# Kernel tuning notes

Hardware: AMD Instinct MI355X
Metric: run time of the kernel (lower is better)

Reference implementation:

```python
import jax, jax.numpy as jnp
from jax import lax
import numpy as np

INPUT_DIMS = 512
HIDDEN_DIMS = 1024
OUTPUT_DIMS = 512
BATCH = 64
T = 256


def setup_inputs() -> dict:
    key = jax.random.key(0)
    ks = jax.random.split(key, 9)
    s_ih = 1.0 / np.sqrt(HIDDEN_DIMS)
    inp = {
        "x": jax.random.normal(ks[0], (BATCH, INPUT_DIMS, T), dtype=jnp.float32),
        # LSTMCell params (PyTorch gate order: i, f, g, o)
        "W_ih": jax.random.uniform(ks[1], (4 * HIDDEN_DIMS, INPUT_DIMS), minval=-s_ih, maxval=s_ih, dtype=jnp.float32),
        "W_hh": jax.random.uniform(ks[2], (4 * HIDDEN_DIMS, HIDDEN_DIMS), minval=-s_ih, maxval=s_ih, dtype=jnp.float32),
        "b_ih": jax.random.uniform(ks[3], (4 * HIDDEN_DIMS,), minval=-s_ih, maxval=s_ih, dtype=jnp.float32),
        "b_hh": jax.random.uniform(ks[4], (4 * HIDDEN_DIMS,), minval=-s_ih, maxval=s_ih, dtype=jnp.float32),
        # Output linear
        "W_out": jax.random.uniform(ks[5], (OUTPUT_DIMS, HIDDEN_DIMS), minval=-s_ih, maxval=s_ih, dtype=jnp.float32),
        "b_out": jax.random.uniform(ks[6], (OUTPUT_DIMS,), minval=-s_ih, maxval=s_ih, dtype=jnp.float32),
        # Initial state (learned-ish constants in the original, sampled from randn)
        "h0": jax.random.normal(ks[7], (1, HIDDEN_DIMS), dtype=jnp.float32),
        "c0": jax.random.normal(ks[8], (1, HIDDEN_DIMS), dtype=jnp.float32),
    }
    return inp


def reference(x, W_ih, W_hh, b_ih, b_hh, W_out, b_out, h0, c0):
    B, I, Tlen = x.shape
    H = W_hh.shape[1]
    h = jnp.broadcast_to(h0, (B, H))
    c = jnp.broadcast_to(c0, (B, H))
    xs = jnp.transpose(x, (2, 0, 1))  # [T, B, I]
    # Precompute the input projection for all timesteps in one GEMM.
    x_proj = jnp.einsum("tbi,gi->tbg", xs, W_ih) + b_ih  # [T, B, 4H]

    def step(carry, xp):
        h, c = carry
        gates = xp + h @ W_hh.T + b_hh  # [B, 4H]
        i_g, f_g, g_g, o_g = jnp.split(gates, 4, axis=-1)
        i_g = jax.nn.sigmoid(i_g)
        f_g = jax.nn.sigmoid(f_g)
        g_g = jnp.tanh(g_g)
        o_g = jax.nn.sigmoid(o_g)
        c_new = f_g * c + i_g * g_g
        h_new = o_g * jnp.tanh(c_new)
        # NOTE: original applies the output head to the CELL state c, not h.
        p = jax.nn.softmax(c_new @ W_out.T + b_out, axis=1)  # [B, O]
        return (h_new, c_new), p

    _, ps = lax.scan(step, (h, c), x_proj)  # ps: [T, B, O]
    # torch.cat along dim 0 per timestep == stack then flatten first two dims.
    return ps.reshape(Tlen * B, -1)
```

## Files before the change

kernel.cpp:

```cpp
#include <hip/hip_runtime.h>


#define T_ 256

typedef __attribute__((ext_vector_type(8))) short bf16x8;
typedef __attribute__((ext_vector_type(4))) float floatx4;
typedef __attribute__((ext_vector_type(4))) int intx4;

__device__ __forceinline__ unsigned short f2bf(float f) {
  unsigned u = __builtin_bit_cast(unsigned, f);
  u += 0x7FFFu + ((u >> 16) & 1u);
  return (unsigned short)(u >> 16);
}

__device__ __forceinline__ float sigm(float x) { return 1.0f / (1.0f + __expf(-x)); }
__device__ __forceinline__ float tanh_fast(float x) {
  return __builtin_fmaf(2.f, sigm(2.f * x), -1.f);
}

__global__ void cvt_w(const float* __restrict__ w, unsigned short* __restrict__ o) {
  const size_t g = (size_t)blockIdx.x * 256 + threadIdx.x;
  const float* s = w + g * 8;
  bf16x8 v;
#pragma unroll
  for (int i = 0; i < 8; ++i) v[i] = (short)f2bf(s[i]);
  *(bf16x8*)(o + g * 8) = v;
}

__global__ void transpose_x(const float* __restrict__ x, unsigned short* __restrict__ xT) {
  __shared__ float tile[32][33];
  const int b = blockIdx.z, i0 = blockIdx.y * 32, t0 = blockIdx.x * 32;
  const int tx = threadIdx.x & 31, ty = threadIdx.x >> 5;
#pragma unroll
  for (int p = 0; p < 4; ++p) {
    const int i = ty + p * 8;
    tile[i][tx] = x[((size_t)b * 512 + i0 + i) * 256 + t0 + tx];
  }
  __syncthreads();
#pragma unroll
  for (int p = 0; p < 4; ++p) {
    const int t = ty + p * 8;
    xT[((size_t)(t0 + t) * 64 + b) * 512 + i0 + tx] = f2bf(tile[tx][t]);
  }
}

__global__ __launch_bounds__(512, 1) void lstm_rec(
    const float* __restrict__ Whh, const float* __restrict__ Wih,
    const float* __restrict__ bih, const float* __restrict__ bhh,
    const float* __restrict__ h0, const float* __restrict__ c0,
    const unsigned short* __restrict__ xT,
    unsigned short* __restrict__ hbuf,
    unsigned short* __restrict__ call)
{
  const int tid = threadIdx.x;
  const int lane = tid & 63;
  const int wv = tid >> 6;
  const int nh = wv & 1, kq = wv >> 1;
  const int mg = blockIdx.x & 3, ng = blockIdx.x >> 2;
  const int l15 = lane & 15, lq = lane >> 4;
  const int row = mg * 16 + l15;

  __shared__ unsigned short hlds[16 * 1032];
  __shared__ float gpart[4][16][66];

  bf16x8 bfrag[2][12];
#pragma unroll
  for (int nt = 0; nt < 2; ++nt) {
    const int ncol = (2 * nh + nt) * 1024 + ng * 16 + l15;
#pragma unroll
    for (int ks = 0; ks < 12; ++ks) {
      const int kg = kq * 384 + ks * 32 + lq * 8;
      const float* s = (kg < 1024) ? (Whh + (size_t)ncol * 1024 + kg)
                                   : (Wih + (size_t)ncol * 512 + (kg - 1024));
      bf16x8 v;
#pragma unroll
      for (int i = 0; i < 8; ++i) v[i] = (short)f2bf(s[i]);
      bfrag[nt][ks] = v;
    }
  }

  const int m_loc = tid >> 4, j = tid & 15;
  const int row_g = mg * 16 + m_loc;
  const int unit = ng * 16 + j;
  float c_reg = 0.f, bs0 = 0.f, bs1 = 0.f, bs2 = 0.f, bs3 = 0.f;
  if (tid < 256) {
    c_reg = c0[unit];
    bs0 = bih[unit] + bhh[unit];
    bs1 = bih[1024 + unit] + bhh[1024 + unit];
    bs2 = bih[2048 + unit] + bhh[2048 + unit];
    bs3 = bih[3072 + unit] + bhh[3072 + unit];
  }

  for (int t = 0; t < T_; ++t) {
    const unsigned short* bx = xT + ((size_t)t * 64 + row) * 512;
    floatx4 zero = {0.f, 0.f, 0.f, 0.f};
    floatx4 acc0 = zero, acc1 = zero;

#pragma unroll
    for (int ks = 0; ks < 12; ++ks) {
      const int kg = kq * 384 + ks * 32 + lq * 8;
      if (kg >= 1024) {
        const bf16x8 af = *(const bf16x8*)(bx + (kg - 1024));
        acc0 = __builtin_amdgcn_mfma_f32_16x16x32_bf16(af, bfrag[0][ks], acc0, 0, 0, 0);
        acc1 = __builtin_amdgcn_mfma_f32_16x16x32_bf16(af, bfrag[1][ks], acc1, 0, 0, 0);
      }
    }

    if (t == 0) {
#pragma unroll
      for (int p = 0; p < 4; ++p) {
        const int e = tid + p * 512;
        const int r = e >> 7, col = (e & 127) * 8;
        const float* s = h0 + col;
        bf16x8 v;
#pragma unroll
        for (int i = 0; i < 8; ++i) v[i] = (short)f2bf(s[i]);
        *(bf16x8*)(hlds + r * 1032 + col) = v;
      }
      __syncthreads();
    } else {
      const unsigned short* hprev = hbuf + ((t + 1) & 1) * 65536;
      const unsigned tagpat = (((t - 1) >> 1) & 1) ? 0x40004000u : 0u;

      if (wv == 0) {
        const unsigned short* ssrc = hprev + (size_t)(mg * 16) * 1024 + (size_t)lane * 16;
        while (true) {
          intx4 s0;
          asm volatile("global_load_dwordx4 %0, %1, off sc0 sc1\n\ts_waitcnt vmcnt(0)"
                       : "=v"(s0) : "v"(ssrc) : "memory");
          unsigned bad = 0;
#pragma unroll
          for (int d = 0; d < 4; ++d) bad |= ((unsigned)s0[d] ^ tagpat) & 0x40004000u;
          if (__all(bad == 0)) break;
          __builtin_amdgcn_s_sleep(1);
        }
      }
      __syncthreads();

      const unsigned short* gsrc = hprev + (size_t)(mg * 16) * 1024 + (size_t)tid * 8;
      intx4 a0, a1, a2, a3;
      while (true) {
        asm volatile(
            "global_load_dwordx4 %0, %4, off sc0 sc1\n\t"
            "global_load_dwordx4 %1, %5, off sc0 sc1\n\t"
            "global_load_dwordx4 %2, %6, off sc0 sc1\n\t"
            "global_load_dwordx4 %3, %7, off sc0 sc1\n\t"
            "s_waitcnt vmcnt(0)"
            : "=v"(a0), "=v"(a1), "=v"(a2), "=v"(a3)
            : "v"(gsrc), "v"(gsrc + 4096), "v"(gsrc + 8192), "v"(gsrc + 12288)
            : "memory");
        unsigned bad = 0;
#pragma unroll
        for (int d = 0; d < 4; ++d) {
          bad |= ((unsigned)a0[d] ^ tagpat) & 0x40004000u;
          bad |= ((unsigned)a1[d] ^ tagpat) & 0x40004000u;
          bad |= ((unsigned)a2[d] ^ tagpat) & 0x40004000u;
          bad |= ((unsigned)a3[d] ^ tagpat) & 0x40004000u;
        }
        if (!bad) break;
        __builtin_amdgcn_s_sleep(1);
      }
      intx4 av[4] = {a0, a1, a2, a3};
#pragma unroll
      for (int p = 0; p < 4; ++p) {
        intx4 v = av[p];
#pragma unroll
        for (int d = 0; d < 4; ++d) v[d] &= (int)0xBFFFBFFFu;
        const int e = tid + p * 512;
        const int r = e >> 7, col = (e & 127) * 8;
        *(intx4*)(hlds + r * 1032 + col) = v;
      }
      __syncthreads();
    }

#pragma unroll
    for (int ks = 0; ks < 12; ++ks) {
      const int kg = kq * 384 + ks * 32 + lq * 8;
      if (kg < 1024) {
        const bf16x8 af = *(const bf16x8*)(hlds + l15 * 1032 + kg);
        acc0 = __builtin_amdgcn_mfma_f32_16x16x32_bf16(af, bfrag[0][ks], acc0, 0, 0, 0);
        acc1 = __builtin_amdgcn_mfma_f32_16x16x32_bf16(af, bfrag[1][ks], acc1, 0, 0, 0);
      }
    }

#pragma unroll
    for (int r = 0; r < 4; ++r) {
      gpart[kq][lq * 4 + r][(2 * nh) * 16 + l15]     = acc0[r];
      gpart[kq][lq * 4 + r][(2 * nh + 1) * 16 + l15] = acc1[r];
    }
    __syncthreads();

    if (tid < 256) {
      float gi = bs0, gf = bs1, gg = bs2, go = bs3;
#pragma unroll
      for (int q = 0; q < 4; ++q) {
        gi += gpart[q][m_loc][j];
        gf += gpart[q][m_loc][16 + j];
        gg += gpart[q][m_loc][32 + j];
        go += gpart[q][m_loc][48 + j];
      }
      const float iv = sigm(gi), fv = sigm(gf), gv = tanh_fast(gg), ov = sigm(go);
      c_reg = fv * c_reg + iv * gv;
      const float hv = ov * tanh_fast(c_reg);

      const unsigned hb = (unsigned)f2bf(hv) | ((unsigned)((t >> 1) & 1) << 14);
      const int base = lane & 56;
      intx4 pk;
#pragma unroll
      for (int k = 0; k < 4; ++k) {
        const unsigned lo = (unsigned)__shfl((int)hb, base + 2 * k, 64) & 0xFFFFu;
        const unsigned hi = (unsigned)__shfl((int)hb, base + 2 * k + 1, 64);
        pk[k] = (int)(lo | (hi << 16));
      }
      if ((tid & 7) == 0) {
        unsigned short* hp = hbuf + (t & 1) * 65536 + row_g * 1024 + (unit & ~7);
        asm volatile("global_store_dwordx4 %0, %1, off sc0 sc1"
                     :: "v"(hp), "v"(pk) : "memory");
      }
      call[((size_t)t * 64 + row_g) * 1024 + unit] = f2bf(c_reg);
    }
  }
}

__global__ __launch_bounds__(256, 1) void lstm_head(
    const unsigned short* __restrict__ call,
    const unsigned short* __restrict__ wout,
    const float* __restrict__ bout,
    float* __restrict__ out)
{
  const int tb = blockIdx.x;
  const int lane = threadIdx.x & 63;
  const int wv = threadIdx.x >> 6;
  const int l15 = lane & 15, lq = lane >> 4;

  __shared__ float sred[2][4][64];

  floatx4 zero = {0.f, 0.f, 0.f, 0.f};
  floatx4 acc[4][8];
#pragma unroll
  for (int mt = 0; mt < 4; ++mt)
#pragma unroll
    for (int nt = 0; nt < 8; ++nt) acc[mt][nt] = zero;

  const unsigned short* abase = call + ((size_t)tb * 64 + l15) * 1024 + lq * 8;
  const unsigned short* bbase = wout + ((size_t)(wv * 128 + l15)) * 1024 + lq * 8;

#pragma unroll 2
  for (int ks = 0; ks < 32; ++ks) {
    bf16x8 a[4];
#pragma unroll
    for (int mt = 0; mt < 4; ++mt)
      a[mt] = *(const bf16x8*)(abase + (size_t)mt * 16 * 1024 + ks * 32);
#pragma unroll
    for (int nt = 0; nt < 8; ++nt) {
      const bf16x8 b = *(const bf16x8*)(bbase + (size_t)nt * 16 * 1024 + ks * 32);
#pragma unroll
      for (int mt = 0; mt < 4; ++mt)
        acc[mt][nt] = __builtin_amdgcn_mfma_f32_16x16x32_bf16(a[mt], b, acc[mt][nt], 0, 0, 0);
    }
  }

#pragma unroll
  for (int nt = 0; nt < 8; ++nt) {
    const float bo = bout[wv * 128 + nt * 16 + l15];
#pragma unroll
    for (int mt = 0; mt < 4; ++mt)
#pragma unroll
      for (int r = 0; r < 4; ++r) acc[mt][nt][r] += bo;
  }

  float rmax[4][4];
#pragma unroll
  for (int mt = 0; mt < 4; ++mt)
#pragma unroll
    for (int r = 0; r < 4; ++r) {
      float m = acc[mt][0][r];
#pragma unroll
      for (int nt = 1; nt < 8; ++nt) m = fmaxf(m, acc[mt][nt][r]);
      m = fmaxf(m, __shfl_xor(m, 1, 64));
      m = fmaxf(m, __shfl_xor(m, 2, 64));
      m = fmaxf(m, __shfl_xor(m, 4, 64));
      m = fmaxf(m, __shfl_xor(m, 8, 64));
      rmax[mt][r] = m;
    }
  if (l15 == 0) {
#pragma unroll
    for (int mt = 0; mt < 4; ++mt)
#pragma unroll
      for (int r = 0; r < 4; ++r) sred[0][wv][mt * 16 + lq * 4 + r] = rmax[mt][r];
  }
  __syncthreads();
  float gmax[4][4], rsum[4][4];
#pragma unroll
  for (int mt = 0; mt < 4; ++mt)
#pragma unroll
    for (int r = 0; r < 4; ++r) {
      const int rw = mt * 16 + lq * 4 + r;
      gmax[mt][r] = fmaxf(fmaxf(sred[0][0][rw], sred[0][1][rw]),
                          fmaxf(sred[0][2][rw], sred[0][3][rw]));
      rsum[mt][r] = 0.f;
    }
#pragma unroll
  for (int mt = 0; mt < 4; ++mt)
#pragma unroll
    for (int nt = 0; nt < 8; ++nt)
#pragma unroll
      for (int r = 0; r < 4; ++r) {
        const float e = __expf(acc[mt][nt][r] - gmax[mt][r]);
        acc[mt][nt][r] = e;
        rsum[mt][r] += e;
      }
#pragma unroll
  for (int mt = 0; mt < 4; ++mt)
#pragma unroll
    for (int r = 0; r < 4; ++r) {
      float s = rsum[mt][r];
      s += __shfl_xor(s, 1, 64);
      s += __shfl_xor(s, 2, 64);
      s += __shfl_xor(s, 4, 64);
      s += __shfl_xor(s, 8, 64);
      rsum[mt][r] = s;
    }
  if (l15 == 0) {
#pragma unroll
    for (int mt = 0; mt < 4; ++mt)
#pragma unroll
      for (int r = 0; r < 4; ++r) sred[1][wv][mt * 16 + lq * 4 + r] = rsum[mt][r];
  }
  __syncthreads();
#pragma unroll
  for (int mt = 0; mt < 4; ++mt)
#pragma unroll
    for (int r = 0; r < 4; ++r) {
      const int rw = mt * 16 + lq * 4 + r;
      const float inv = 1.0f / (sred[1][0][rw] + sred[1][1][rw] +
                                sred[1][2][rw] + sred[1][3][rw]);
      float* orow = out + ((size_t)tb * 64 + rw) * 512 + wv * 128 + l15;
#pragma unroll
      for (int nt = 0; nt < 8; ++nt) orow[nt * 16] = acc[mt][nt][r] * inv;
    }
}

extern "C" void kernel_launch(void* const* d_in, const int* in_sizes, int n_in,
                              void* d_out, int out_size, void* d_ws, size_t ws_size,
                              hipStream_t stream) {
  const float* x    = (const float*)d_in[0];
  const float* Wih  = (const float*)d_in[1];
  const float* Whh  = (const float*)d_in[2];
  const float* bih  = (const float*)d_in[3];
  const float* bhh  = (const float*)d_in[4];
  const float* Wout = (const float*)d_in[5];
  const float* bout = (const float*)d_in[6];
  const float* h0   = (const float*)d_in[7];
  const float* c0   = (const float*)d_in[8];
  float* out = (float*)d_out;

  char* ws = (char*)d_ws;
  unsigned short* hbuf  = (unsigned short*)(ws + 4096);
  unsigned short* woutb = (unsigned short*)(ws + 266240);
  unsigned short* xT    = (unsigned short*)(ws + 1314816);
  unsigned short* call  = (unsigned short*)(ws + 18092032);

  hipMemsetAsync(hbuf, 0xFF, 262144, stream);
  cvt_w<<<256, 256, 0, stream>>>(Wout, woutb);
  transpose_x<<<dim3(8, 16, 64), 256, 0, stream>>>(x, xT);
  lstm_rec<<<256, 512, 0, stream>>>(Whh, Wih, bih, bhh, h0, c0, xT, hbuf, call);
  lstm_head<<<256, 256, 0, stream>>>(call, woutb, bout, out);
}
```

Measured before the change: 1.316 ms.

## Use per-timestep hidden-state ring buffer to avoid tagged double-buffer polling

Adds a mode that writes each timestep's hidden state to its own slot in a 256-entry ring buffer, pre-filled with 0xFF, so readiness is detected by cleared tag bits rather than alternating parity tags. The bulk read now uses plain cached loads, and only chunks that are not yet valid are re-polled with coherent loads. This is meant to cut the cost of the cross-block barrier on each step, in exchange for a 32 MB memset and extra workspace. The old path is kept as a fallback when the workspace is too small.

Measured after the change: 1.219 ms. 1.08x faster.

```diff
diff --git a/kernel.cpp b/kernel.cpp
--- a/kernel.cpp
+++ b/kernel.cpp
@@ -50,7 +50,9 @@
     const float* __restrict__ h0, const float* __restrict__ c0,
     const unsigned short* __restrict__ xT,
     unsigned short* __restrict__ hbuf,
-    unsigned short* __restrict__ call)
+    unsigned short* __restrict__ hring,
+    unsigned short* __restrict__ call,
+    const int mode)
 {
   const int tid = threadIdx.x;
   const int lane = tid & 63;
@@ -118,10 +120,8 @@
         *(bf16x8*)(hlds + r * 1032 + col) = v;
       }
       __syncthreads();
-    } else {
-      const unsigned short* hprev = hbuf + ((t + 1) & 1) * 65536;
-      const unsigned tagpat = (((t - 1) >> 1) & 1) ? 0x40004000u : 0u;
-
+    } else if (mode) {
+      const unsigned short* hprev = hring + (size_t)(t - 1) * 65536;
       if (wv == 0) {
         const unsigned short* ssrc = hprev + (size_t)(mg * 16) * 1024 + (size_t)lane * 16;
         while (true) {
@@ -130,13 +130,58 @@
                        : "=v"(s0) : "v"(ssrc) : "memory");
           unsigned bad = 0;
 #pragma unroll
+          for (int d = 0; d < 4; ++d) bad |= (unsigned)s0[d] & 0x40004000u;
+          if (__all(bad == 0)) break;
+          __builtin_amdgcn_s_sleep(1);
+        }
+      }
+      __syncthreads();
+      const unsigned short* gsrc = hprev + (size_t)(mg * 16) * 1024 + (size_t)tid * 8;
+      intx4 av[4];
+      av[0] = *(const intx4*)(gsrc);
+      av[1] = *(const intx4*)(gsrc + 4096);
+      av[2] = *(const intx4*)(gsrc + 8192);
+      av[3] = *(const intx4*)(gsrc + 12288);
+#pragma unroll
+      for (int p = 0; p < 4; ++p) {
+        unsigned bad = 0;
+#pragma unroll
+        for (int d = 0; d < 4; ++d) bad |= (unsigned)av[p][d] & 0x40004000u;
+        if (bad) {
+          const unsigned short* ptr = gsrc + p * 4096;
+          while (true) {
+            intx4 vv;
+            asm volatile("global_load_dwordx4 %0, %1, off sc0 sc1\n\ts_waitcnt vmcnt(0)"
+                         : "=v"(vv) : "v"(ptr) : "memory");
+            unsigned b2 = 0;
+#pragma unroll
+            for (int d = 0; d < 4; ++d) b2 |= (unsigned)vv[d] & 0x40004000u;
+            if (!b2) { av[p] = vv; break; }
+            __builtin_amdgcn_s_sleep(1);
+          }
+        }
+        const int e = tid + p * 512;
+        const int r = e >> 7, col = (e & 127) * 8;
+        *(intx4*)(hlds + r * 1032 + col) = av[p];
+      }
+      __syncthreads();
+    } else {
+      const unsigned short* hprev = hbuf + ((t + 1) & 1) * 65536;
+      const unsigned tagpat = (((t - 1) >> 1) & 1) ? 0x40004000u : 0u;
+      if (wv == 0) {
+        const unsigned short* ssrc = hprev + (size_t)(mg * 16) * 1024 + (size_t)lane * 16;
+        while (true) {
+          intx4 s0;
+          asm volatile("global_load_dwordx4 %0, %1, off sc0 sc1\n\ts_waitcnt vmcnt(0)"
+                       : "=v"(s0) : "v"(ssrc) : "memory");
+          unsigned bad = 0;
+#pragma unroll
           for (int d = 0; d < 4; ++d) bad |= ((unsigned)s0[d] ^ tagpat) & 0x40004000u;
           if (__all(bad == 0)) break;
           __builtin_amdgcn_s_sleep(1);
         }
       }
       __syncthreads();
-
       const unsigned short* gsrc = hprev + (size_t)(mg * 16) * 1024 + (size_t)tid * 8;
       intx4 a0, a1, a2, a3;
       while (true) {
@@ -160,10 +205,10 @@
         if (!bad) break;
         __builtin_amdgcn_s_sleep(1);
       }
-      intx4 av[4] = {a0, a1, a2, a3};
+      intx4 avv[4] = {a0, a1, a2, a3};
 #pragma unroll
       for (int p = 0; p < 4; ++p) {
-        intx4 v = av[p];
+        intx4 v = avv[p];
 #pragma unroll
         for (int d = 0; d < 4; ++d) v[d] &= (int)0xBFFFBFFFu;
         const int e = tid + p * 512;
@@ -203,7 +248,8 @@
       c_reg = fv * c_reg + iv * gv;
       const float hv = ov * tanh_fast(c_reg);
 
-      const unsigned hb = (unsigned)f2bf(hv) | ((unsigned)((t >> 1) & 1) << 14);
+      const unsigned hb = (unsigned)f2bf(hv)
+                        | (mode ? 0u : ((unsigned)((t >> 1) & 1) << 14));
       const int base = lane & 56;
       intx4 pk;
 #pragma unroll
@@ -213,7 +259,9 @@
         pk[k] = (int)(lo | (hi << 16));
       }
       if ((tid & 7) == 0) {
-        unsigned short* hp = hbuf + (t & 1) * 65536 + row_g * 1024 + (unit & ~7);
+        unsigned short* hp = (mode ? hring + (size_t)t * 65536
+                                   : hbuf + (t & 1) * 65536)
+                             + row_g * 1024 + (unit & ~7);
         asm volatile("global_store_dwordx4 %0, %1, off sc0 sc1"
                      :: "v"(hp), "v"(pk) : "memory");
       }
@@ -360,10 +408,18 @@
   unsigned short* woutb = (unsigned short*)(ws + 266240);
   unsigned short* xT    = (unsigned short*)(ws + 1314816);
   unsigned short* call  = (unsigned short*)(ws + 18092032);
-
-  hipMemsetAsync(hbuf, 0xFF, 262144, stream);
+  unsigned short* hring = (unsigned short*)(ws + 51646464);
+
+  const size_t need = 51646464ull + 33554432ull;
+  const int mode = (ws_size >= need) ? 1 : 0;
+
+  if (mode) {
+    hipMemsetAsync(hring, 0xFF, 33554432, stream);
+  } else {
+    hipMemsetAsync(hbuf, 0xFF, 262144, stream);
+  }
   cvt_w<<<256, 256, 0, stream>>>(Wout, woutb);
   transpose_x<<<dim3(8, 16, 64), 256, 0, stream>>>(x, xT);
-  lstm_rec<<<256, 512, 0, stream>>>(Whh, Wih, bih, bhh, h0, c0, xT, hbuf, call);
+  lstm_rec<<<256, 512, 0, stream>>>(Whh, Wih, bih, bhh, h0, c0, xT, hbuf, hring, call, mode);
   lstm_head<<<256, 256, 0, stream>>>(call, woutb, bout, out);
 }
```

## Repartition recurrence blocks into 8-row groups and add per-step h ring buffer

Applied to the files above, without the earlier changes.

Each block now covers 8 batch rows and 32 hidden units, so every block reads only 8 rows of h per step instead of 16. Each step's h is also written to a per-timestep ring buffer that starts filled with 0xFF, which lets readers poll without tag parity and with a cheaper sc0-only load. The old double-buffered, tagged path stays as a fallback when the workspace is too small or after repeated polling misses. The cost is an extra 32 MB memset, extra global stores every step, half of each MFMA's output rows left unused, and doubled B-fragment register use.

Result: slower. 2.168 ms (+64.8%).

```diff
diff --git a/kernel.cpp b/kernel.cpp
--- a/kernel.cpp
+++ b/kernel.cpp
@@ -2,6 +2,7 @@
 
 
 #define T_ 256
+#define FASTROUNDS 48
 
 typedef __attribute__((ext_vector_type(8))) short bf16x8;
 typedef __attribute__((ext_vector_type(4))) float floatx4;
@@ -50,38 +51,42 @@
     const float* __restrict__ h0, const float* __restrict__ c0,
     const unsigned short* __restrict__ xT,
     unsigned short* __restrict__ hbuf,
-    unsigned short* __restrict__ call)
+    unsigned short* __restrict__ hring,
+    unsigned short* __restrict__ call,
+    const int have_ring)
 {
   const int tid = threadIdx.x;
   const int lane = tid & 63;
   const int wv = tid >> 6;
   const int nh = wv & 1, kq = wv >> 1;
-  const int mg = blockIdx.x & 3, ng = blockIdx.x >> 2;
+  const int xg = blockIdx.x & 7;
+  const int ngb = blockIdx.x >> 3;
   const int l15 = lane & 15, lq = lane >> 4;
-  const int row = mg * 16 + l15;
-
-  __shared__ unsigned short hlds[16 * 1032];
-  __shared__ float gpart[4][16][66];
-
-  bf16x8 bfrag[2][12];
-#pragma unroll
-  for (int nt = 0; nt < 2; ++nt) {
-    const int ncol = (2 * nh + nt) * 1024 + ng * 16 + l15;
+  const int hrow = l15 & 7;
+
+  __shared__ unsigned short hlds[8 * 1032];
+  __shared__ float gpart[4][8][132];
+
+  bf16x8 bfrag[4][12];
+#pragma unroll
+  for (int a = 0; a < 4; ++a) {
+    const int c = nh * 64 + a * 16 + l15;
+    const int wcol = (c >> 5) * 1024 + ngb * 32 + (c & 31);
 #pragma unroll
     for (int ks = 0; ks < 12; ++ks) {
       const int kg = kq * 384 + ks * 32 + lq * 8;
-      const float* s = (kg < 1024) ? (Whh + (size_t)ncol * 1024 + kg)
-                                   : (Wih + (size_t)ncol * 512 + (kg - 1024));
+      const float* s = (kg < 1024) ? (Whh + (size_t)wcol * 1024 + kg)
+                                   : (Wih + (size_t)wcol * 512 + (kg - 1024));
       bf16x8 v;
 #pragma unroll
       for (int i = 0; i < 8; ++i) v[i] = (short)f2bf(s[i]);
-      bfrag[nt][ks] = v;
-    }
-  }
-
-  const int m_loc = tid >> 4, j = tid & 15;
-  const int row_g = mg * 16 + m_loc;
-  const int unit = ng * 16 + j;
+      bfrag[a][ks] = v;
+    }
+  }
+
+  const int m_loc = tid >> 5, j = tid & 31;
+  const int row_g = xg * 8 + m_loc;
+  const int unit = ngb * 32 + j;
   float c_reg = 0.f, bs0 = 0.f, bs1 = 0.f, bs2 = 0.f, bs3 = 0.f;
   if (tid < 256) {
     c_reg = c0[unit];
@@ -91,102 +96,95 @@
     bs3 = bih[3072 + unit] + bhh[3072 + unit];
   }
 
+  int fails = have_ring ? 0 : 1000;
+
   for (int t = 0; t < T_; ++t) {
-    const unsigned short* bx = xT + ((size_t)t * 64 + row) * 512;
     floatx4 zero = {0.f, 0.f, 0.f, 0.f};
-    floatx4 acc0 = zero, acc1 = zero;
-
+    floatx4 acc[4] = {zero, zero, zero, zero};
+
+    const unsigned short* bx = xT + ((size_t)t * 64 + xg * 8 + hrow) * 512;
 #pragma unroll
     for (int ks = 0; ks < 12; ++ks) {
       const int kg = kq * 384 + ks * 32 + lq * 8;
       if (kg >= 1024) {
         const bf16x8 af = *(const bf16x8*)(bx + (kg - 1024));
-        acc0 = __builtin_amdgcn_mfma_f32_16x16x32_bf16(af, bfrag[0][ks], acc0, 0, 0, 0);
-        acc1 = __builtin_amdgcn_mfma_f32_16x16x32_bf16(af, bfrag[1][ks], acc1, 0, 0, 0);
+#pragma unroll
+        for (int a = 0; a < 4; ++a)
+          acc[a] = __builtin_amdgcn_mfma_f32_16x16x32_bf16(af, bfrag[a][ks], acc[a], 0, 0, 0);
       }
     }
 
     if (t == 0) {
 #pragma unroll
-      for (int p = 0; p < 4; ++p) {
-        const int e = tid + p * 512;
-        const int r = e >> 7, col = (e & 127) * 8;
-        const float* s = h0 + col;
+      for (int p = 0; p < 2; ++p) {
+        const int g = tid + p * 512;
+        const int row8 = g >> 7, colu = (g & 127) * 8;
+        const float* s = h0 + colu;
         bf16x8 v;
 #pragma unroll
         for (int i = 0; i < 8; ++i) v[i] = (short)f2bf(s[i]);
-        *(bf16x8*)(hlds + r * 1032 + col) = v;
-      }
-      __syncthreads();
+        *(bf16x8*)(hlds + row8 * 1032 + colu) = v;
+      }
     } else {
-      const unsigned short* hprev = hbuf + ((t + 1) & 1) * 65536;
-      const unsigned tagpat = (((t - 1) >> 1) & 1) ? 0x40004000u : 0u;
-
-      if (wv == 0) {
-        const unsigned short* ssrc = hprev + (size_t)(mg * 16) * 1024 + (size_t)lane * 16;
-        while (true) {
-          intx4 s0;
-          asm volatile("global_load_dwordx4 %0, %1, off sc0 sc1\n\ts_waitcnt vmcnt(0)"
-                       : "=v"(s0) : "v"(ssrc) : "memory");
-          unsigned bad = 0;
-#pragma unroll
-          for (int d = 0; d < 4; ++d) bad |= ((unsigned)s0[d] ^ tagpat) & 0x40004000u;
-          if (__all(bad == 0)) break;
-          __builtin_amdgcn_s_sleep(1);
+      const int rt = t - 1;
+      const unsigned tagpat = ((rt >> 1) & 1) ? 0x40004000u : 0u;
+#pragma unroll
+      for (int p = 0; p < 2; ++p) {
+        const int g = tid + p * 512;
+        const int row8 = g >> 7, colu = (g & 127) * 8;
+        const unsigned short* rp =
+            hring + ((size_t)(rt * 8 + xg) * 8 + row8) * 1024 + colu;
+        const unsigned short* mp =
+            hbuf + ((t + 1) & 1) * 65536 + (size_t)(xg * 8 + row8) * 1024 + colu;
+        intx4 v;
+        bool got = false;
+        if (fails < 4) {
+          for (int r = 0; r < FASTROUNDS; ++r) {
+            asm volatile("global_load_dwordx4 %0, %1, off sc0\n\ts_waitcnt vmcnt(0)"
+                         : "=v"(v) : "v"(rp) : "memory");
+            unsigned bad = 0;
+#pragma unroll
+            for (int d = 0; d < 4; ++d) bad |= (unsigned)v[d] & 0x40004000u;
+            if (!bad) { got = true; break; }
+            __builtin_amdgcn_s_sleep(1);
+          }
         }
-      }
-      __syncthreads();
-
-      const unsigned short* gsrc = hprev + (size_t)(mg * 16) * 1024 + (size_t)tid * 8;
-      intx4 a0, a1, a2, a3;
-      while (true) {
-        asm volatile(
-            "global_load_dwordx4 %0, %4, off sc0 sc1\n\t"
-            "global_load_dwordx4 %1, %5, off sc0 sc1\n\t"
-            "global_load_dwordx4 %2, %6, off sc0 sc1\n\t"
-            "global_load_dwordx4 %3, %7, off sc0 sc1\n\t"
-            "s_waitcnt vmcnt(0)"
-            : "=v"(a0), "=v"(a1), "=v"(a2), "=v"(a3)
-            : "v"(gsrc), "v"(gsrc + 4096), "v"(gsrc + 8192), "v"(gsrc + 12288)
-            : "memory");
-        unsigned bad = 0;
-#pragma unroll
-        for (int d = 0; d < 4; ++d) {
-          bad |= ((unsigned)a0[d] ^ tagpat) & 0x40004000u;
-          bad |= ((unsigned)a1[d] ^ tagpat) & 0x40004000u;
-          bad |= ((unsigned)a2[d] ^ tagpat) & 0x40004000u;
-          bad |= ((unsigned)a3[d] ^ tagpat) & 0x40004000u;
+        if (!got) {
+          if (fails < 1000) ++fails;
+          while (true) {
+            asm volatile("global_load_dwordx4 %0, %1, off sc0 sc1\n\ts_waitcnt vmcnt(0)"
+                         : "=v"(v) : "v"(mp) : "memory");
+            unsigned bad = 0;
+#pragma unroll
+            for (int d = 0; d < 4; ++d) bad |= ((unsigned)v[d] ^ tagpat) & 0x40004000u;
+            if (!bad) break;
+            __builtin_amdgcn_s_sleep(1);
+          }
+#pragma unroll
+          for (int d = 0; d < 4; ++d) v[d] &= (int)0xBFFFBFFFu;
         }
-        if (!bad) break;
-        __builtin_amdgcn_s_sleep(1);
-      }
-      intx4 av[4] = {a0, a1, a2, a3};
-#pragma unroll
-      for (int p = 0; p < 4; ++p) {
-        intx4 v = av[p];
-#pragma unroll
-        for (int d = 0; d < 4; ++d) v[d] &= (int)0xBFFFBFFFu;
-        const int e = tid + p * 512;
-        const int r = e >> 7, col = (e & 127) * 8;
-        *(intx4*)(hlds + r * 1032 + col) = v;
-      }
-      __syncthreads();
-    }
+        *(intx4*)(hlds + row8 * 1032 + colu) = v;
+      }
+    }
+    __syncthreads();
 
 #pragma unroll
     for (int ks = 0; ks < 12; ++ks) {
       const int kg = kq * 384 + ks * 32 + lq * 8;
       if (kg < 1024) {
-        const bf16x8 af = *(const bf16x8*)(hlds + l15 * 1032 + kg);
-        acc0 = __builtin_amdgcn_mfma_f32_16x16x32_bf16(af, bfrag[0][ks], acc0, 0, 0, 0);
-        acc1 = __builtin_amdgcn_mfma_f32_16x16x32_bf16(af, bfrag[1][ks], acc1, 0, 0, 0);
-      }
-    }
-
-#pragma unroll
-    for (int r = 0; r < 4; ++r) {
-      gpart[kq][lq * 4 + r][(2 * nh) * 16 + l15]     = acc0[r];
-      gpart[kq][lq * 4 + r][(2 * nh + 1) * 16 + l15] = acc1[r];
+        const bf16x8 af = *(const bf16x8*)(hlds + hrow * 1032 + kg);
+#pragma unroll
+        for (int a = 0; a < 4; ++a)
+          acc[a] = __builtin_amdgcn_mfma_f32_16x16x32_bf16(af, bfrag[a][ks], acc[a], 0, 0, 0);
+      }
+    }
+
+    if (lq < 2) {
+#pragma unroll
+      for (int a = 0; a < 4; ++a)
+#pragma unroll
+        for (int r = 0; r < 4; ++r)
+          gpart[kq][lq * 4 + r][nh * 64 + a * 16 + l15] = acc[a][r];
     }
     __syncthreads();
 
@@ -195,15 +193,15 @@
 #pragma unroll
       for (int q = 0; q < 4; ++q) {
         gi += gpart[q][m_loc][j];
-        gf += gpart[q][m_loc][16 + j];
-        gg += gpart[q][m_loc][32 + j];
-        go += gpart[q][m_loc][48 + j];
+        gf += gpart[q][m_loc][32 + j];
+        gg += gpart[q][m_loc][64 + j];
+        go += gpart[q][m_loc][96 + j];
       }
       const float iv = sigm(gi), fv = sigm(gf), gv = tanh_fast(gg), ov = sigm(go);
       c_reg = fv * c_reg + iv * gv;
       const float hv = ov * tanh_fast(c_reg);
 
-      const unsigned hb = (unsigned)f2bf(hv) | ((unsigned)((t >> 1) & 1) << 14);
+      const unsigned hb = (unsigned)f2bf(hv);
       const int base = lane & 56;
       intx4 pk;
 #pragma unroll
@@ -213,9 +211,17 @@
         pk[k] = (int)(lo | (hi << 16));
       }
       if ((tid & 7) == 0) {
-        unsigned short* hp = hbuf + (t & 1) * 65536 + row_g * 1024 + (unit & ~7);
+        const int u8 = unit & ~7;
+        if (have_ring) {
+          *(intx4*)(hring + ((size_t)(t * 8 + xg) * 8 + m_loc) * 1024 + u8) = pk;
+        }
+        const unsigned tagmask = ((t >> 1) & 1) ? 0x40004000u : 0u;
+        intx4 pk2;
+#pragma unroll
+        for (int k = 0; k < 4; ++k) pk2[k] = pk[k] | (int)tagmask;
+        unsigned short* hp = hbuf + (t & 1) * 65536 + row_g * 1024 + u8;
         asm volatile("global_store_dwordx4 %0, %1, off sc0 sc1"
-                     :: "v"(hp), "v"(pk) : "memory");
+                     :: "v"(hp), "v"(pk2) : "memory");
       }
       call[((size_t)t * 64 + row_g) * 1024 + unit] = f2bf(c_reg);
     }
@@ -360,10 +366,15 @@
   unsigned short* woutb = (unsigned short*)(ws + 266240);
   unsigned short* xT    = (unsigned short*)(ws + 1314816);
   unsigned short* call  = (unsigned short*)(ws + 18092032);
+  unsigned short* hring = (unsigned short*)(ws + 51646464);
+
+  const size_t need = 51646464ull + 33554432ull;
+  const int have_ring = (ws_size >= need) ? 1 : 0;
 
   hipMemsetAsync(hbuf, 0xFF, 262144, stream);
+  if (have_ring) hipMemsetAsync(hring, 0xFF, 33554432, stream);
   cvt_w<<<256, 256, 0, stream>>>(Wout, woutb);
   transpose_x<<<dim3(8, 16, 64), 256, 0, stream>>>(x, xT);
-  lstm_rec<<<256, 512, 0, stream>>>(Whh, Wih, bih, bhh, h0, c0, xT, hbuf, call);
+  lstm_rec<<<256, 512, 0, stream>>>(Whh, Wih, bih, bhh, h0, c0, xT, hbuf, hring, call, have_ring);
   lstm_head<<<256, 256, 0, stream>>>(call, woutb, bout, out);
 }
```
